# Kernel optimization log

Hardware: AMD Instinct MI355X
Metric: run time of the kernel (lower is better)

## Reference

```python
import jax, jax.numpy as jnp
import numpy as np

EPS = 1e-06

def _gcn_layer(x, adj, d_inv_sqrt, W, b):
    # adj_norm = D^-1/2 A D^-1/2; apply as row/col scaling (same math as diag matmuls)
    adj_norm = d_inv_sqrt[:, None] * adj * d_inv_sqrt[None, :]
    h = adj_norm @ x              # [N, F] dense aggregation
    return h @ W + b              # linear


def setup_inputs() -> dict:
    key = jax.random.key(0)
    k1, k2, k3, k4, k5, k6 = jax.random.split(key, 6)
    N, F_in, F_hid, F_out = 8192, 128, 64, 2
    x = jax.random.normal(k1, (N, F_in), dtype=jnp.float32)
    adj = jax.random.uniform(k2, (N, N), dtype=jnp.float32)
    # nn.Linear default init: U(-1/sqrt(fan_in), 1/sqrt(fan_in))
    s1 = 1.0 / np.sqrt(F_in)
    s2 = 1.0 / np.sqrt(F_hid)
    W1 = jax.random.uniform(k3, (F_in, F_hid), dtype=jnp.float32, minval=-s1, maxval=s1)
    b1 = jax.random.uniform(k4, (F_hid,), dtype=jnp.float32, minval=-s1, maxval=s1)
    W2 = jax.random.uniform(k5, (F_hid, F_out), dtype=jnp.float32, minval=-s2, maxval=s2)
    b2 = jax.random.uniform(k6, (F_out,), dtype=jnp.float32, minval=-s2, maxval=s2)
    return {"x": x, "adj": adj, "W1": W1, "b1": b1, "W2": W2, "b2": b2}


def reference(x, adj, W1, b1, W2, b2):
    d_inv_sqrt = 1.0 / jnp.sqrt(adj.sum(axis=1) + EPS)   # [N]
    h = jax.nn.relu(_gcn_layer(x, adj, d_inv_sqrt, W1, b1))
    out = _gcn_layer(h, adj, d_inv_sqrt, W2, b2)
    return out
```

## Files before the change

kernel.cpp:

```cpp
#include <hip/hip_runtime.h>

#define NN 8192
typedef unsigned short u16;
typedef __attribute__((ext_vector_type(8))) short short8;
typedef __attribute__((ext_vector_type(4))) float f32x4;

__device__ __forceinline__ u16 f2bf(float f) {
    unsigned u = __builtin_bit_cast(unsigned, f);
    return (u16)((u + 0x7FFFu + ((u >> 16) & 1u)) >> 16);
}
__device__ __forceinline__ float bf2f(u16 u) {
    unsigned v = ((unsigned)u) << 16;
    return __builtin_bit_cast(float, v);
}
__device__ __forceinline__ void split3(float v, u16& h, u16& m, u16& l) {
    h = f2bf(v);
    float r1 = v - bf2f(h);
    m = f2bf(r1);
    float r2 = r1 - bf2f(m);
    l = f2bf(r2);
}

__global__ __launch_bounds__(256) void k1(const float* __restrict__ adj, double* __restrict__ d) {
    int row = blockIdx.x * 4 + (threadIdx.x >> 6);
    int l = threadIdx.x & 63;
    const float4* r = (const float4*)(adj + (size_t)row * NN) + l;
    double s = 0.0;
#pragma unroll 8
    for (int it = 0; it < 32; ++it) {
        float4 v = r[(size_t)it * 64];
        s += (double)v.x + (double)v.y + (double)v.z + (double)v.w;
    }
#pragma unroll
    for (int o = 32; o > 0; o >>= 1) s += __shfl_down(s, o);
    if (l == 0) d[row] = 1.0 / sqrt(s + 1e-6);
}

__global__ __launch_bounds__(256) void k2s(const float* __restrict__ x, const float* __restrict__ W1,
                                           const double* __restrict__ d, u16* __restrict__ Ph,
                                           u16* __restrict__ Pm, u16* __restrict__ Pl) {
    __shared__ float sw[128 * 64];
    __shared__ float sx[32 * 128];
    int tid = threadIdx.x;
    int jb = blockIdx.x * 32;
#pragma unroll
    for (int o = 0; o < 8; ++o)
        ((float4*)sw)[tid * 8 + o] = ((const float4*)W1)[tid * 8 + o];
#pragma unroll
    for (int o = 0; o < 4; ++o)
        ((float4*)sx)[tid * 4 + o] = ((const float4*)(x + (size_t)jb * 128))[tid * 4 + o];
    __syncthreads();
    int f = tid & 63, g = tid >> 6;
    double acc[8] = {};
    for (int c = 0; c < 128; ++c) {
        double w = (double)sw[c * 64 + f];
#pragma unroll
        for (int rr = 0; rr < 8; ++rr)
            acc[rr] += (double)sx[(g * 8 + rr) * 128 + c] * w;
    }
    short8 hv, mv, lv;
#pragma unroll
    for (int rr = 0; rr < 8; ++rr) {
        int j = jb + g * 8 + rr;
        float v = (float)(acc[rr] * d[j]);
        u16 hh, mm, ll;
        split3(v, hh, mm, ll);
        hv[rr] = (short)hh; mv[rr] = (short)mm; lv[rr] = (short)ll;
    }
    size_t off = (size_t)f * NN + jb + g * 8;
    *(short8*)(Ph + off) = hv;
    *(short8*)(Pm + off) = mv;
    *(short8*)(Pl + off) = lv;
}

__global__ __launch_bounds__(256) void k3s(const float* __restrict__ adj, const u16* __restrict__ Ph,
                                           const u16* __restrict__ Pm, const u16* __restrict__ Pl,
                                           float* __restrict__ part, int kspl, int klen) {
    int tid = threadIdx.x;
    int w = tid >> 6, l = tid & 63, q = l >> 4, n = l & 15;
    int outer = blockIdx.x / kspl, ks = blockIdx.x - outer * kspl;
    int rb = outer * 128 + w * 32;
    int k0 = ks * klen;
    f32x4 acc[2][4] = {};
    const float* a0 = adj + (size_t)(rb + n) * NN + k0 + q * 8;
    const float* a1 = a0 + (size_t)16 * NN;
    for (int kt = 0; kt < klen; kt += 32) {
        short8 ah[2], am[2], al[2];
#pragma unroll
        for (int rt = 0; rt < 2; ++rt) {
            const float* ap = (rt ? a1 : a0) + kt;
            float4 f0 = *(const float4*)ap;
            float4 f1 = *(const float4*)(ap + 4);
            float vv[8] = {f0.x, f0.y, f0.z, f0.w, f1.x, f1.y, f1.z, f1.w};
#pragma unroll
            for (int e = 0; e < 8; ++e) {
                u16 hh, mm, ll;
                split3(vv[e], hh, mm, ll);
                ah[rt][e] = (short)hh; am[rt][e] = (short)mm; al[rt][e] = (short)ll;
            }
        }
#pragma unroll
        for (int nt = 0; nt < 4; ++nt) {
            size_t boff = (size_t)(nt * 16 + n) * NN + k0 + kt + q * 8;
            short8 bh = *(const short8*)(Ph + boff);
            short8 bm = *(const short8*)(Pm + boff);
            short8 bl = *(const short8*)(Pl + boff);
#pragma unroll
            for (int rt = 0; rt < 2; ++rt) {
                f32x4 c = acc[rt][nt];
                c = __builtin_amdgcn_mfma_f32_16x16x32_bf16(ah[rt], bh, c, 0, 0, 0);
                c = __builtin_amdgcn_mfma_f32_16x16x32_bf16(ah[rt], bm, c, 0, 0, 0);
                c = __builtin_amdgcn_mfma_f32_16x16x32_bf16(am[rt], bh, c, 0, 0, 0);
                c = __builtin_amdgcn_mfma_f32_16x16x32_bf16(ah[rt], bl, c, 0, 0, 0);
                c = __builtin_amdgcn_mfma_f32_16x16x32_bf16(am[rt], bm, c, 0, 0, 0);
                c = __builtin_amdgcn_mfma_f32_16x16x32_bf16(al[rt], bh, c, 0, 0, 0);
                acc[rt][nt] = c;
            }
        }
    }
    float* pb = part + (size_t)ks * NN * 64;
#pragma unroll
    for (int rt = 0; rt < 2; ++rt)
#pragma unroll
        for (int nt = 0; nt < 4; ++nt)
#pragma unroll
            for (int r = 0; r < 4; ++r)
                pb[(size_t)(rb + rt * 16 + q * 4 + r) * 64 + nt * 16 + n] = acc[rt][nt][r];
}

__global__ __launch_bounds__(256) void k3r(const float* __restrict__ part, const double* __restrict__ d,
                                           const float* __restrict__ b1, const float* __restrict__ W2,
                                           float* __restrict__ q, int kspl) {
    int row = blockIdx.x * 4 + (threadIdx.x >> 6);
    int f = threadIdx.x & 63;
    double acc = 0.0;
    for (int ks = 0; ks < kspl; ++ks)
        acc += (double)part[((size_t)ks * NN + row) * 64 + f];
    double di = d[row];
    double h = di * acc + (double)b1[f];
    h = h > 0.0 ? h : 0.0;
    double t0 = h * (double)W2[f * 2 + 0];
    double t1 = h * (double)W2[f * 2 + 1];
#pragma unroll
    for (int o = 32; o > 0; o >>= 1) {
        t0 += __shfl_down(t0, o);
        t1 += __shfl_down(t1, o);
    }
    if (f == 0) {
        q[(size_t)row * 2 + 0] = (float)(di * t0);
        q[(size_t)row * 2 + 1] = (float)(di * t1);
    }
}

__global__ __launch_bounds__(256) void k4(const float* __restrict__ adj, const float* __restrict__ q,
                                          const double* __restrict__ d, const float* __restrict__ b2,
                                          float* __restrict__ out) {
    int row = blockIdx.x * 4 + (threadIdx.x >> 6);
    int l = threadIdx.x & 63;
    const float4* a = (const float4*)(adj + (size_t)row * NN) + l;
    const float4* qv = (const float4*)q;
    double acc0 = 0.0, acc1 = 0.0;
#pragma unroll 4
    for (int it = 0; it < 32; ++it) {
        float4 av = a[(size_t)it * 64];
        size_t jv = ((size_t)it * 64 + l) * 2;
        float4 qa = qv[jv];
        float4 qb = qv[jv + 1];
        acc0 += (double)av.x * qa.x + (double)av.y * qa.z + (double)av.z * qb.x + (double)av.w * qb.z;
        acc1 += (double)av.x * qa.y + (double)av.y * qa.w + (double)av.z * qb.y + (double)av.w * qb.w;
    }
#pragma unroll
    for (int o = 32; o > 0; o >>= 1) {
        acc0 += __shfl_down(acc0, o);
        acc1 += __shfl_down(acc1, o);
    }
    if (l == 0) {
        double di = d[row];
        out[(size_t)row * 2 + 0] = (float)(di * acc0 + (double)b2[0]);
        out[(size_t)row * 2 + 1] = (float)(di * acc1 + (double)b2[1]);
    }
}

__global__ __launch_bounds__(256) void k2f(const float* __restrict__ x, const float* __restrict__ W1,
                                           const double* __restrict__ d, float* __restrict__ P) {
    __shared__ float sw[128 * 64];
    __shared__ float sx[16 * 128];
    int tid = threadIdx.x;
    int jb = blockIdx.x * 16;
#pragma unroll
    for (int o = 0; o < 8; ++o)
        ((float4*)sw)[tid * 8 + o] = ((const float4*)W1)[tid * 8 + o];
#pragma unroll
    for (int o = 0; o < 2; ++o)
        ((float4*)sx)[tid * 2 + o] = ((const float4*)(x + (size_t)jb * 128))[tid * 2 + o];
    __syncthreads();
    int f = tid & 63, g = tid >> 6;
    double acc[4] = {};
    for (int c = 0; c < 128; ++c) {
        double w = (double)sw[c * 64 + f];
#pragma unroll
        for (int rr = 0; rr < 4; ++rr)
            acc[rr] += (double)sx[(g * 4 + rr) * 128 + c] * w;
    }
#pragma unroll
    for (int rr = 0; rr < 4; ++rr) {
        int j = jb + g * 4 + rr;
        P[(size_t)j * 64 + f] = (float)(acc[rr] * d[j]);
    }
}
__global__ __launch_bounds__(256) void k3f(const float* __restrict__ adj, const float* __restrict__ P,
                                           const double* __restrict__ d, const float* __restrict__ b1,
                                           const float* __restrict__ W2, float* __restrict__ q) {
    __shared__ float sp[128 * 64];
    __shared__ float sa[16 * 128];
    int tid = threadIdx.x;
    int f = tid & 63, g = tid >> 6;
    int rb = blockIdx.x * 16;
    double acc[4] = {};
    for (int ch = 0; ch < 64; ++ch) {
        __syncthreads();
#pragma unroll
        for (int o = 0; o < 8; ++o)
            ((float4*)sp)[tid * 8 + o] = ((const float4*)(P + (size_t)ch * 128 * 64))[tid * 8 + o];
#pragma unroll
        for (int o = 0; o < 2; ++o) {
            int t = tid * 2 + o;
            int r = t >> 5, cv = t & 31;
            ((float4*)(sa + r * 128))[cv] = *(const float4*)(adj + (size_t)(rb + r) * NN + ch * 128 + cv * 4);
        }
        __syncthreads();
        const float* sar = sa + g * 4 * 128;
        for (int jj = 0; jj < 128; jj += 4) {
            float4 a0 = *(const float4*)(sar + jj);
            float4 a1 = *(const float4*)(sar + 128 + jj);
            float4 a2 = *(const float4*)(sar + 256 + jj);
            float4 a3 = *(const float4*)(sar + 384 + jj);
            double p0 = (double)sp[(jj + 0) * 64 + f];
            double p1 = (double)sp[(jj + 1) * 64 + f];
            double p2 = (double)sp[(jj + 2) * 64 + f];
            double p3 = (double)sp[(jj + 3) * 64 + f];
            acc[0] += (double)a0.x * p0 + (double)a0.y * p1 + (double)a0.z * p2 + (double)a0.w * p3;
            acc[1] += (double)a1.x * p0 + (double)a1.y * p1 + (double)a1.z * p2 + (double)a1.w * p3;
            acc[2] += (double)a2.x * p0 + (double)a2.y * p1 + (double)a2.z * p2 + (double)a2.w * p3;
            acc[3] += (double)a3.x * p0 + (double)a3.y * p1 + (double)a3.z * p2 + (double)a3.w * p3;
        }
    }
    double w0 = (double)W2[f * 2 + 0], w1 = (double)W2[f * 2 + 1], bb = (double)b1[f];
#pragma unroll
    for (int rr = 0; rr < 4; ++rr) {
        int row = rb + g * 4 + rr;
        double di = d[row];
        double h = di * acc[rr] + bb;
        h = h > 0.0 ? h : 0.0;
        double t0 = h * w0, t1 = h * w1;
#pragma unroll
        for (int o = 32; o > 0; o >>= 1) {
            t0 += __shfl_down(t0, o);
            t1 += __shfl_down(t1, o);
        }
        if (f == 0) {
            q[(size_t)row * 2 + 0] = (float)(di * t0);
            q[(size_t)row * 2 + 1] = (float)(di * t1);
        }
    }
}

extern "C" void kernel_launch(void* const* d_in, const int* in_sizes, int n_in,
                              void* d_out, int out_size, void* d_ws, size_t ws_size,
                              hipStream_t stream) {
    const float* x   = (const float*)d_in[0];
    const float* adj = (const float*)d_in[1];
    const float* W1  = (const float*)d_in[2];
    const float* b1  = (const float*)d_in[3];
    const float* W2  = (const float*)d_in[4];
    const float* b2  = (const float*)d_in[5];
    float* out = (float*)d_out;

    char* ws = (char*)d_ws;
    double* dvec = (double*)ws;

    int kspl = 0;
    for (int c : {8, 4, 2, 1}) {
        size_t need = 65536 + 3u * 1048576u + (size_t)c * 2097152u + 65536u;
        if (ws_size >= need) { kspl = c; break; }
    }

    k1<<<2048, 256, 0, stream>>>(adj, dvec);
    if (kspl > 0) {
        u16* Ph = (u16*)(ws + 65536);
        u16* Pm = Ph + (size_t)64 * NN;
        u16* Pl = Pm + (size_t)64 * NN;
        float* part = (float*)(ws + 65536 + 3u * 1048576u);
        float* q = (float*)(ws + 65536 + 3u * 1048576u + (size_t)kspl * 2097152u);
        k2s<<<256, 256, 0, stream>>>(x, W1, dvec, Ph, Pm, Pl);
        k3s<<<64 * kspl, 256, 0, stream>>>(adj, Ph, Pm, Pl, part, kspl, NN / kspl);
        k3r<<<2048, 256, 0, stream>>>(part, dvec, b1, W2, q, kspl);
        k4<<<2048, 256, 0, stream>>>(adj, q, dvec, b2, out);
    } else {
        float* P = (float*)(ws + 65536);
        float* q = (float*)(ws + 65536 + 2097152);
        k2f<<<512, 256, 0, stream>>>(x, W1, dvec, P);
        k3f<<<512, 256, 0, stream>>>(adj, P, dvec, b1, W2, q);
        k4<<<2048, 256, 0, stream>>>(adj, q, dvec, b2, out);
    }
}
```

Before: 557.3 us.

## Shrink k3s row tile to 16 per wave, double grid, allow 16-way K split

The split-bf16 MFMA aggregation kernel now gives each wave 16 rows instead of 32 and launches twice as many blocks. The K-split factor may rise to 16 when the workspace allows, so more blocks run in parallel and each needs fewer registers. In exchange, each loaded B fragment (Ph/Pm/Pl) is reused over half as many rows, which doubles that traffic, and k3r must reduce more partial sums. The degree and layer-2 loops also split their double-precision accumulations into independent chains to shorten dependency latency.

```diff
diff --git a/kernel.cpp b/kernel.cpp
--- a/kernel.cpp
+++ b/kernel.cpp
@@ -25,12 +25,13 @@
     int row = blockIdx.x * 4 + (threadIdx.x >> 6);
     int l = threadIdx.x & 63;
     const float4* r = (const float4*)(adj + (size_t)row * NN) + l;
-    double s = 0.0;
+    double s0 = 0.0, s1 = 0.0, s2 = 0.0, s3 = 0.0;
 #pragma unroll 8
     for (int it = 0; it < 32; ++it) {
         float4 v = r[(size_t)it * 64];
-        s += (double)v.x + (double)v.y + (double)v.z + (double)v.w;
-    }
+        s0 += (double)v.x; s1 += (double)v.y; s2 += (double)v.z; s3 += (double)v.w;
+    }
+    double s = (s0 + s1) + (s2 + s3);
 #pragma unroll
     for (int o = 32; o > 0; o >>= 1) s += __shfl_down(s, o);
     if (l == 0) d[row] = 1.0 / sqrt(s + 1e-6);
@@ -79,25 +80,20 @@
     int tid = threadIdx.x;
     int w = tid >> 6, l = tid & 63, q = l >> 4, n = l & 15;
     int outer = blockIdx.x / kspl, ks = blockIdx.x - outer * kspl;
-    int rb = outer * 128 + w * 32;
+    int rb = outer * 64 + w * 16;
     int k0 = ks * klen;
-    f32x4 acc[2][4] = {};
+    f32x4 acc[4] = {};
     const float* a0 = adj + (size_t)(rb + n) * NN + k0 + q * 8;
-    const float* a1 = a0 + (size_t)16 * NN;
     for (int kt = 0; kt < klen; kt += 32) {
-        short8 ah[2], am[2], al[2];
-#pragma unroll
-        for (int rt = 0; rt < 2; ++rt) {
-            const float* ap = (rt ? a1 : a0) + kt;
-            float4 f0 = *(const float4*)ap;
-            float4 f1 = *(const float4*)(ap + 4);
-            float vv[8] = {f0.x, f0.y, f0.z, f0.w, f1.x, f1.y, f1.z, f1.w};
-#pragma unroll
-            for (int e = 0; e < 8; ++e) {
-                u16 hh, mm, ll;
-                split3(vv[e], hh, mm, ll);
-                ah[rt][e] = (short)hh; am[rt][e] = (short)mm; al[rt][e] = (short)ll;
-            }
+        float4 f0 = *(const float4*)(a0 + kt);
+        float4 f1 = *(const float4*)(a0 + kt + 4);
+        float vv[8] = {f0.x, f0.y, f0.z, f0.w, f1.x, f1.y, f1.z, f1.w};
+        short8 ah, am, al;
+#pragma unroll
+        for (int e = 0; e < 8; ++e) {
+            u16 hh, mm, ll;
+            split3(vv[e], hh, mm, ll);
+            ah[e] = (short)hh; am[e] = (short)mm; al[e] = (short)ll;
         }
 #pragma unroll
         for (int nt = 0; nt < 4; ++nt) {
@@ -105,27 +101,22 @@
             short8 bh = *(const short8*)(Ph + boff);
             short8 bm = *(const short8*)(Pm + boff);
             short8 bl = *(const short8*)(Pl + boff);
-#pragma unroll
-            for (int rt = 0; rt < 2; ++rt) {
-                f32x4 c = acc[rt][nt];
-                c = __builtin_amdgcn_mfma_f32_16x16x32_bf16(ah[rt], bh, c, 0, 0, 0);
-                c = __builtin_amdgcn_mfma_f32_16x16x32_bf16(ah[rt], bm, c, 0, 0, 0);
-                c = __builtin_amdgcn_mfma_f32_16x16x32_bf16(am[rt], bh, c, 0, 0, 0);
-                c = __builtin_amdgcn_mfma_f32_16x16x32_bf16(ah[rt], bl, c, 0, 0, 0);
-                c = __builtin_amdgcn_mfma_f32_16x16x32_bf16(am[rt], bm, c, 0, 0, 0);
-                c = __builtin_amdgcn_mfma_f32_16x16x32_bf16(al[rt], bh, c, 0, 0, 0);
-                acc[rt][nt] = c;
-            }
+            f32x4 c = acc[nt];
+            c = __builtin_amdgcn_mfma_f32_16x16x32_bf16(ah, bh, c, 0, 0, 0);
+            c = __builtin_amdgcn_mfma_f32_16x16x32_bf16(ah, bm, c, 0, 0, 0);
+            c = __builtin_amdgcn_mfma_f32_16x16x32_bf16(am, bh, c, 0, 0, 0);
+            c = __builtin_amdgcn_mfma_f32_16x16x32_bf16(ah, bl, c, 0, 0, 0);
+            c = __builtin_amdgcn_mfma_f32_16x16x32_bf16(am, bm, c, 0, 0, 0);
+            c = __builtin_amdgcn_mfma_f32_16x16x32_bf16(al, bh, c, 0, 0, 0);
+            acc[nt] = c;
         }
     }
     float* pb = part + (size_t)ks * NN * 64;
 #pragma unroll
-    for (int rt = 0; rt < 2; ++rt)
-#pragma unroll
-        for (int nt = 0; nt < 4; ++nt)
-#pragma unroll
-            for (int r = 0; r < 4; ++r)
-                pb[(size_t)(rb + rt * 16 + q * 4 + r) * 64 + nt * 16 + n] = acc[rt][nt][r];
+    for (int nt = 0; nt < 4; ++nt)
+#pragma unroll
+        for (int r = 0; r < 4; ++r)
+            pb[(size_t)(rb + q * 4 + r) * 64 + nt * 16 + n] = acc[nt][r];
 }
 
 __global__ __launch_bounds__(256) void k3r(const float* __restrict__ part, const double* __restrict__ d,
@@ -166,8 +157,8 @@
         size_t jv = ((size_t)it * 64 + l) * 2;
         float4 qa = qv[jv];
         float4 qb = qv[jv + 1];
-        acc0 += (double)av.x * qa.x + (double)av.y * qa.z + (double)av.z * qb.x + (double)av.w * qb.z;
-        acc1 += (double)av.x * qa.y + (double)av.y * qa.w + (double)av.z * qb.y + (double)av.w * qb.w;
+        acc0 += ((double)av.x * qa.x + (double)av.y * qa.z) + ((double)av.z * qb.x + (double)av.w * qb.z);
+        acc1 += ((double)av.x * qa.y + (double)av.y * qa.w) + ((double)av.z * qb.y + (double)av.w * qb.w);
     }
 #pragma unroll
     for (int o = 32; o > 0; o >>= 1) {
@@ -280,7 +271,7 @@
     double* dvec = (double*)ws;
 
     int kspl = 0;
-    for (int c : {8, 4, 2, 1}) {
+    for (int c : {16, 8, 4, 2, 1}) {
         size_t need = 65536 + 3u * 1048576u + (size_t)c * 2097152u + 65536u;
         if (ws_size >= need) { kspl = c; break; }
     }
@@ -293,7 +284,7 @@
         float* part = (float*)(ws + 65536 + 3u * 1048576u);
         float* q = (float*)(ws + 65536 + 3u * 1048576u + (size_t)kspl * 2097152u);
         k2s<<<256, 256, 0, stream>>>(x, W1, dvec, Ph, Pm, Pl);
-        k3s<<<64 * kspl, 256, 0, stream>>>(adj, Ph, Pm, Pl, part, kspl, NN / kspl);
+        k3s<<<128 * kspl, 256, 0, stream>>>(adj, Ph, Pm, Pl, part, kspl, NN / kspl);
         k3r<<<2048, 256, 0, stream>>>(part, dvec, b1, W2, q, kspl);
         k4<<<2048, 256, 0, stream>>>(adj, q, dvec, b2, out);
     } else {
```

New measurement: 638.7 us. 1.15x slower.
